# Kernel optimization log

Measured on AMD Instinct MI355X. Metric: run time of the kernel, lower is better.

## Reference

```python
import jax, jax.numpy as jnp
import numpy as np

SIM_T = 32  # simulation_length


def uniform_spikes(rates, T):
    """Faithful port of to_uniform_spikes, vectorized over all T cycles.
    rates: (B, D) in [0,1] -> spike train (T, B, D) of {0,1} floats."""
    N = jnp.round(rates * T).astype(jnp.int32)          # (B, D)
    cycles = jnp.arange(T, dtype=jnp.float32)[:, None, None]  # (T,1,1)
    N_safe = jnp.maximum(N, 1)
    spacing = T / N_safe.astype(jnp.float32)
    mask = (N != 0) & (N != T)                          # cycle < T always holds here
    res = mask & (jnp.floor(cycles / spacing) < N_safe) & (jnp.floor(jnp.mod(cycles, spacing)) == 0)
    res = res.astype(jnp.float32)
    res = jnp.where(N == T, jnp.float32(1.0), res)      # result[N == T] = 1.0
    return res


def lif_core(spikes_in, weight, threshold):
    """LIF integration: memb += inp @ W.T; fired = threshold < memb; Default reset.
    spikes_in: (T, B, in); weight: (out, in). Returns (T, B, out) spike train."""
    B = spikes_in.shape[1]
    out_dim = weight.shape[0]

    def step(memb, s):
        memb = memb + s @ weight.T
        fired = threshold < memb                        # thresholding_mode '<'
        memb = jnp.where(fired, memb - threshold, memb) # firing_mode 'Default'
        return memb, fired.astype(jnp.float32)

    _, out_train = jax.lax.scan(step, jnp.zeros((B, out_dim), spikes_in.dtype), spikes_in)
    return out_train


def setup_inputs() -> dict:
    key = jax.random.key(0)
    k = jax.random.split(key, 8)
    B, D_in = 64, 4096
    x = jax.random.uniform(k[0], (B, D_in), dtype=jnp.float32)          # rates in [0,1]
    w0 = jax.random.normal(k[1], (4096, 4096), dtype=jnp.float32) / np.sqrt(4096.0)
    t0 = jnp.float32(1.0)
    w2 = jax.random.normal(k[2], (1000, 1024), dtype=jnp.float32) / np.sqrt(1024.0)
    t2 = jnp.float32(1.0)
    idx0 = jax.random.permutation(k[3], 4096).astype(jnp.int32)
    idx1 = jax.random.permutation(k[4], 4096).astype(jnp.int32)
    idx2 = jax.random.permutation(k[5], 1024).astype(jnp.int32)
    idx_out = jnp.arange(1000, dtype=jnp.int32)
    return {"x": x, "w0": w0, "t0": t0, "w2": w2, "t2": t2,
            "idx0": idx0, "idx1": idx1, "idx2": idx2, "idx_out": idx_out}


def reference(x, w0, t0, w2, t2, idx0, idx1, idx2, idx_out):
    B = x.shape[0]
    T = SIM_T
    # Input encoding (Uniform spike mode), train shape (T, B, 4096)
    inp_train = uniform_spikes(x, T)
    # NeuralCore 0: per-source gather + LIF
    s0 = lif_core(inp_train[:, :, idx0], w0, t0)        # (T, B, 4096)
    # ComputeOp avg_pool2d: sync barrier -> rates over full window
    rates = s0[:, :, idx1].mean(axis=0)                 # (B, 4096)
    C, H, W = 64, 8, 8
    xr = rates.reshape(B, C, H, W)
    pooled = xr.reshape(B, C, H // 2, 2, W // 2, 2).mean(axis=(3, 5))  # (B, 64, 4, 4)
    y_rates = jnp.clip(pooled.reshape(B, -1), 0.0, 1.0) # (B, 1024)
    s1 = uniform_spikes(y_rates, T)                     # (T, B, 1024)
    # NeuralCore 2
    s2 = lif_core(s1[:, :, idx2], w2, t2)               # (T, B, 1000)
    # Output accumulation over cycles (spike counts)
    return s2[:, :, idx_out].sum(axis=0)                # (B, 1000)
```

## Files before the change

kernel.cpp:

```cpp
#include <hip/hip_runtime.h>
#include <stdint.h>
#include <stddef.h>

#define D0 4096
#define D1 1024
#define NOUT 1000
#define NB 64
#define PD0 4352
#define PD1 1264

constexpr uint32_t spike_pattern_ct(int N) {
  if (N <= 0) return 0u;
  if (N >= 32) return 0xFFFFFFFFu;
  float sp = 32.0f / (float)N;
  uint32_t m = 0;
  for (int c = 0; c < 32; ++c) {
    double q = (double)c / (double)sp;
    int n = (int)q;
    double r = (double)c - (double)n * (double)sp;
    if (r < 1.0) m |= (1u << c);
  }
  return m;
}

__global__ void transpose_w0_k(const float* __restrict__ w, float* __restrict__ wt) {
  __shared__ float tile[32][33];
  int j0 = blockIdx.x * 32;
  int o0 = blockIdx.y * 32;
  int tx = threadIdx.x, ty = threadIdx.y;
  float4 v = *reinterpret_cast<const float4*>(&w[(size_t)(o0 + ty) * D0 + j0 + 4 * tx]);
  tile[ty][4 * tx + 0] = v.x;
  tile[ty][4 * tx + 1] = v.y;
  tile[ty][4 * tx + 2] = v.z;
  tile[ty][4 * tx + 3] = v.w;
  __syncthreads();
  float4 u;
  u.x = tile[4 * tx + 0][ty];
  u.y = tile[4 * tx + 1][ty];
  u.z = tile[4 * tx + 2][ty];
  u.w = tile[4 * tx + 3][ty];
  *reinterpret_cast<float4*>(&wt[(size_t)(j0 + ty) * D0 + o0 + 4 * tx]) = u;
}

__global__ void transpose_w2_k(const float* __restrict__ w, float* __restrict__ wt) {
  __shared__ float tile[32][33];
  int j0 = blockIdx.x * 32;
  int o0 = blockIdx.y * 32;
  int tx = threadIdx.x, ty = threadIdx.y;
  int o = o0 + ty;
  float4 v = make_float4(0.f, 0.f, 0.f, 0.f);
  if (o < NOUT) v = *reinterpret_cast<const float4*>(&w[(size_t)o * D1 + j0 + 4 * tx]);
  tile[ty][4 * tx + 0] = v.x;
  tile[ty][4 * tx + 1] = v.y;
  tile[ty][4 * tx + 2] = v.z;
  tile[ty][4 * tx + 3] = v.w;
  __syncthreads();
  float4 u;
  u.x = tile[4 * tx + 0][ty];
  u.y = tile[4 * tx + 1][ty];
  u.z = tile[4 * tx + 2][ty];
  u.w = tile[4 * tx + 3][ty];
  *reinterpret_cast<float4*>(&wt[(size_t)(j0 + ty) * D1 + o0 + 4 * tx]) = u;
}

__global__ void prep_sort0_k(const float* __restrict__ x, const int* __restrict__ idx0,
                             uint16_t* __restrict__ perm, int* __restrict__ starts) {
  __shared__ int keys[D0];
  __shared__ int hist[33];
  __shared__ int base[34];
  __shared__ int cursor[33];
  int b = blockIdx.x;
  int tid = threadIdx.x;
  if (tid < 33) hist[tid] = 0;
  for (int p = tid; p < PD0; p += 256) perm[(size_t)b * PD0 + p] = 0;
  __syncthreads();
  for (int j = tid; j < D0; j += 256) {
    int k = (int)rintf(x[b * D0 + idx0[j]] * 32.0f);
    keys[j] = k;
    atomicAdd(&hist[k], 1);
  }
  __syncthreads();
  if (tid == 0) {
    int s = 0;
    for (int k = 0; k < 33; ++k) {
      base[k] = s; cursor[k] = s;
      s = (s + hist[k] + 7) & ~7;
    }
    base[33] = s;
  }
  __syncthreads();
  if (tid < 34) starts[b * 68 + tid] = base[tid];
  if (tid < 33) starts[b * 68 + 34 + tid] = hist[tid];
  for (int j = tid; j < D0; j += 256) {
    int k = keys[j];
    int pos = atomicAdd(&cursor[k], 1);
    perm[(size_t)b * PD0 + pos] = (uint16_t)j;
  }
}

__global__ void prep_sort1_k(const int* __restrict__ k0, const int* __restrict__ idx1,
                             const int* __restrict__ idx2,
                             uint16_t* __restrict__ perm, int* __restrict__ starts) {
  __shared__ int keys[D1];
  __shared__ int hist[33];
  __shared__ int base[34];
  __shared__ int cursor[33];
  int b = blockIdx.x;
  int tid = threadIdx.x;
  if (tid < 33) hist[tid] = 0;
  for (int p = tid; p < PD1; p += 256) perm[(size_t)b * PD1 + p] = 0;
  __syncthreads();
  for (int j = tid; j < D1; j += 256) {
    int q2 = idx2[j];
    int c = q2 >> 4;
    int h2 = (q2 >> 2) & 3;
    int w2 = q2 & 3;
    int cnt = 0;
#pragma unroll
    for (int dh = 0; dh < 2; ++dh)
#pragma unroll
      for (int dw = 0; dw < 2; ++dw) {
        int q = c * 64 + (2 * h2 + dh) * 8 + (2 * w2 + dw);
        cnt += k0[b * D0 + idx1[q]];
      }
    int k = (int)rintf((float)cnt * 0.25f);
    keys[j] = k;
    atomicAdd(&hist[k], 1);
  }
  __syncthreads();
  if (tid == 0) {
    int s = 0;
    for (int k = 0; k < 33; ++k) {
      base[k] = s; cursor[k] = s;
      s = (s + hist[k] + 7) & ~7;
    }
    base[33] = s;
  }
  __syncthreads();
  if (tid < 34) starts[b * 68 + tid] = base[tid];
  if (tid < 33) starts[b * 68 + 34 + tid] = hist[tid];
  for (int j = tid; j < D1; j += 256) {
    int k = keys[j];
    int pos = atomicAdd(&cursor[k], 1);
    perm[(size_t)b * PD1 + pos] = (uint16_t)j;
  }
}

template <int D, int PD, int OSTRIDE, int TILES>
__launch_bounds__(512, 2)
__global__ void lif_core_k(const float* __restrict__ wt, const uint16_t* __restrict__ perm,
                           const int* __restrict__ starts, const float* __restrict__ thr_p,
                           int* __restrict__ cnt_out) {
  __shared__ double cshare[16][256];
  __shared__ uint16_t permS[PD];
  int tid = threadIdx.x;
  int b = blockIdx.y;
  int col = tid & 255;
  int half = __builtin_amdgcn_readfirstlane(tid >> 8);

  {
    const ushort2* p2 = reinterpret_cast<const ushort2*>(perm + (size_t)b * PD);
    ushort2* s2 = reinterpret_cast<ushort2*>(permS);
    for (int i = tid; i < PD / 2; i += 512) s2[i] = p2[i];
  }
  __syncthreads();

  const int* stA = starts + b * 68;
  const int* stL = starts + b * 68 + 34;
  double th = (double)thr_p[0];

#define RDIDX(P) do { \
    const uint32_t* _q = reinterpret_cast<const uint32_t*>(permS + ip); \
    uint32_t _w0 = _q[0], _w1 = _q[1], _w2 = _q[2], _w3 = _q[3]; \
    uint32_t _s0 = __builtin_amdgcn_readfirstlane(_w0); \
    uint32_t _s1 = __builtin_amdgcn_readfirstlane(_w1); \
    uint32_t _s2 = __builtin_amdgcn_readfirstlane(_w2); \
    uint32_t _s3 = __builtin_amdgcn_readfirstlane(_w3); \
    P##0 = _s0 & 0xffffu; P##1 = _s0 >> 16; \
    P##2 = _s1 & 0xffffu; P##3 = _s1 >> 16; \
    P##4 = _s2 & 0xffffu; P##5 = _s2 >> 16; \
    P##6 = _s3 & 0xffffu; P##7 = _s3 >> 16; \
    ip += 8; \
  } while (0)

#define GATHER(F, P) do { \
    F##0 = wt[(size_t)P##0 * OSTRIDE + o]; \
    F##1 = wt[(size_t)P##1 * OSTRIDE + o]; \
    F##2 = wt[(size_t)P##2 * OSTRIDE + o]; \
    F##3 = wt[(size_t)P##3 * OSTRIDE + o]; \
    F##4 = wt[(size_t)P##4 * OSTRIDE + o]; \
    F##5 = wt[(size_t)P##5 * OSTRIDE + o]; \
    F##6 = wt[(size_t)P##6 * OSTRIDE + o]; \
    F##7 = wt[(size_t)P##7 * OSTRIDE + o]; \
  } while (0)

#define ACC8(F) do { \
    a0 += (double)F##0; a1 += (double)F##1; a2 += (double)F##2; a3 += (double)F##3; \
    a0 += (double)F##4; a1 += (double)F##5; a2 += (double)F##6; a3 += (double)F##7; \
  } while (0)

  for (int zt = 0; zt < TILES; ++zt) {
    int o = (blockIdx.x + gridDim.x * zt) * 256 + col;

    double bs[33];
#pragma unroll
    for (int k = 1; k <= 32; ++k) bs[k] = 0.0;

#pragma unroll
    for (int k = 1; k <= 32; ++k) {
      int hs0 = __builtin_amdgcn_readfirstlane(stA[k]);
      int len = __builtin_amdgcn_readfirstlane(stL[k]);
      if (len == 0) continue;
      int half_lo = ((len >> 1) + 7) & ~7;
      int mid8 = half_lo < len ? half_lo : len;
      int ip  = half ? hs0 + mid8 : hs0;
      int myn = half ? len - mid8 : mid8;
      if (myn == 0) continue;
      int ng = myn >> 3, rem = myn & 7;
      uint32_t pA0, pA1, pA2, pA3, pA4, pA5, pA6, pA7;
      uint32_t pB0, pB1, pB2, pB3, pB4, pB5, pB6, pB7;
      float fA0, fA1, fA2, fA3, fA4, fA5, fA6, fA7;
      float fB0, fB1, fB2, fB3, fB4, fB5, fB6, fB7;
      double a0 = 0.0, a1 = 0.0, a2 = 0.0, a3 = 0.0;
      if (ng > 0) {
        RDIDX(pA); GATHER(fA, pA);
        int g = 1;
        for (; g + 1 < ng; g += 2) {
          RDIDX(pB); GATHER(fB, pB);
          ACC8(fA);
          RDIDX(pA); GATHER(fA, pA);
          ACC8(fB);
        }
        if (g < ng) {
          RDIDX(pB); GATHER(fB, pB);
          ACC8(fA);
          ACC8(fB);
        } else {
          ACC8(fA);
        }
      }
      if (rem) {
        RDIDX(pA); GATHER(fA, pA);
        a0 += (double)fA0;
        if (rem > 1) a1 += (double)fA1;
        if (rem > 2) a2 += (double)fA2;
        if (rem > 3) a3 += (double)fA3;
        if (rem > 4) a0 += (double)fA4;
        if (rem > 5) a1 += (double)fA5;
        if (rem > 6) a2 += (double)fA6;
      }
      bs[k] = (a0 + a1) + (a2 + a3);
    }

    __syncthreads();
    if (half) {
#pragma unroll
      for (int k = 1; k <= 16; ++k) cshare[k - 1][col] = bs[k];
    }
    __syncthreads();
    if (!half) {
#pragma unroll
      for (int k = 1; k <= 16; ++k) bs[k] += cshare[k - 1][col];
    }
    __syncthreads();
    if (half) {
#pragma unroll
      for (int k = 17; k <= 32; ++k) cshare[k - 17][col] = bs[k];
    }
    __syncthreads();
    if (!half) {
#pragma unroll
      for (int k = 17; k <= 32; ++k) bs[k] += cshare[k - 17][col];

      double memb = 0.0;
      int cnt = 0;
#pragma unroll
      for (int t = 0; t < 32; ++t) {
#pragma unroll
        for (int k = 1; k <= 32; ++k)
          if ((spike_pattern_ct(k) >> t) & 1u) memb += bs[k];
        if (memb > th) { memb -= th; ++cnt; }
      }
      cnt_out[(size_t)b * OSTRIDE + o] = cnt;
    }
  }
#undef RDIDX
#undef GATHER
#undef ACC8
}

__global__ void write_out_k(const int* __restrict__ cnt2, const int* __restrict__ idx_out,
                            float* __restrict__ out) {
  int i = blockIdx.x * 256 + threadIdx.x;
  if (i >= NB * NOUT) return;
  int b = i / NOUT;
  int r = i - b * NOUT;
  out[i] = (float)cnt2[b * D1 + idx_out[r]];
}

extern "C" void kernel_launch(void* const* d_in, const int* in_sizes, int n_in,
                              void* d_out, int out_size, void* d_ws, size_t ws_size,
                              hipStream_t stream) {
  const float* x      = (const float*)d_in[0];
  const float* w0     = (const float*)d_in[1];
  const float* t0     = (const float*)d_in[2];
  const float* w2     = (const float*)d_in[3];
  const float* t2     = (const float*)d_in[4];
  const int*   idx0   = (const int*)d_in[5];
  const int*   idx1   = (const int*)d_in[6];
  const int*   idx2   = (const int*)d_in[7];
  const int*   idx_out= (const int*)d_in[8];
  float* out = (float*)d_out;

  char* ws = (char*)d_ws;
  float*    w0T    = (float*)ws;    ws += (size_t)D0 * D0 * 4;
  float*    w2T    = (float*)ws;    ws += (size_t)D1 * D1 * 4;
  uint16_t* perm0  = (uint16_t*)ws; ws += (size_t)NB * PD0 * 2;
  uint16_t* perm2  = (uint16_t*)ws; ws += (size_t)NB * PD1 * 2;
  int*      k0     = (int*)ws;      ws += (size_t)NB * D0 * 4;
  int*      cnt2   = (int*)ws;      ws += (size_t)NB * D1 * 4;
  int*      starts0= (int*)ws;      ws += (size_t)NB * 68 * 4;
  int*      starts2= (int*)ws;      ws += (size_t)NB * 68 * 4;

  transpose_w0_k<<<dim3(D0 / 32, D0 / 32), dim3(8, 32), 0, stream>>>(w0, w0T);
  transpose_w2_k<<<dim3(D1 / 32, D1 / 32), dim3(8, 32), 0, stream>>>(w2, w2T);
  prep_sort0_k<<<NB, 256, 0, stream>>>(x, idx0, perm0, starts0);
  lif_core_k<D0, PD0, D0, 2><<<dim3(8, NB, 1), 512, 0, stream>>>(w0T, perm0, starts0, t0, k0);
  prep_sort1_k<<<NB, 256, 0, stream>>>(k0, idx1, idx2, perm2, starts2);
  lif_core_k<D1, PD1, D1, 1><<<dim3(4, NB, 1), 512, 0, stream>>>(w2T, perm2, starts2, t2, cnt2);
  write_out_k<<<(NB * NOUT + 255) / 256, 256, 0, stream>>>(cnt2, idx_out, out);
}
```

Baseline: 384.9 us.

## Split LIF buckets across four thread groups in 1024-thread blocks

The LIF kernel blocks grow from 512 to 1024 threads, organised as four 256-thread groups. Each group now owns 8 of the 32 spike-count buckets outright, instead of two halves splitting every bucket's index range. Per-thread partial sums shrink from 33 doubles to 8, and the four-barrier two-phase exchange becomes a single shared-memory write. Group 0 then reads the other groups' sums directly from shared memory during the threshold loop. The aim is lower register pressure and more waves in flight for the latency-bound gather, at the cost of load imbalance between groups, larger shared memory, and a very aggressive launch-bounds occupancy hint that may force register spills.

New measurement: 361.6 us. 6.1% less time.

```diff
diff --git a/kernel.cpp b/kernel.cpp
--- a/kernel.cpp
+++ b/kernel.cpp
@@ -147,21 +147,21 @@
 }
 
 template <int D, int PD, int OSTRIDE, int TILES>
-__launch_bounds__(512, 2)
+__launch_bounds__(1024, 8)
 __global__ void lif_core_k(const float* __restrict__ wt, const uint16_t* __restrict__ perm,
                            const int* __restrict__ starts, const float* __restrict__ thr_p,
                            int* __restrict__ cnt_out) {
-  __shared__ double cshare[16][256];
+  __shared__ double cshare[24][256];
   __shared__ uint16_t permS[PD];
   int tid = threadIdx.x;
   int b = blockIdx.y;
   int col = tid & 255;
-  int half = __builtin_amdgcn_readfirstlane(tid >> 8);
+  int g = __builtin_amdgcn_readfirstlane(tid >> 8);
 
   {
     const ushort2* p2 = reinterpret_cast<const ushort2*>(perm + (size_t)b * PD);
     ushort2* s2 = reinterpret_cast<ushort2*>(permS);
-    for (int i = tid; i < PD / 2; i += 512) s2[i] = p2[i];
+    for (int i = tid; i < PD / 2; i += 1024) s2[i] = p2[i];
   }
   __syncthreads();
 
@@ -202,21 +202,18 @@
   for (int zt = 0; zt < TILES; ++zt) {
     int o = (blockIdx.x + gridDim.x * zt) * 256 + col;
 
-    double bs[33];
-#pragma unroll
-    for (int k = 1; k <= 32; ++k) bs[k] = 0.0;
-
-#pragma unroll
-    for (int k = 1; k <= 32; ++k) {
+    double bs[8];
+#pragma unroll
+    for (int i = 0; i < 8; ++i) bs[i] = 0.0;
+
+#pragma unroll
+    for (int i = 0; i < 8; ++i) {
+      int k = 4 * i + g + 1;
       int hs0 = __builtin_amdgcn_readfirstlane(stA[k]);
       int len = __builtin_amdgcn_readfirstlane(stL[k]);
       if (len == 0) continue;
-      int half_lo = ((len >> 1) + 7) & ~7;
-      int mid8 = half_lo < len ? half_lo : len;
-      int ip  = half ? hs0 + mid8 : hs0;
-      int myn = half ? len - mid8 : mid8;
-      if (myn == 0) continue;
-      int ng = myn >> 3, rem = myn & 7;
+      int ip = hs0;
+      int ng = len >> 3, rem = len & 7;
       uint32_t pA0, pA1, pA2, pA3, pA4, pA5, pA6, pA7;
       uint32_t pB0, pB1, pB2, pB3, pB4, pB5, pB6, pB7;
       float fA0, fA1, fA2, fA3, fA4, fA5, fA6, fA7;
@@ -224,14 +221,14 @@
       double a0 = 0.0, a1 = 0.0, a2 = 0.0, a3 = 0.0;
       if (ng > 0) {
         RDIDX(pA); GATHER(fA, pA);
-        int g = 1;
-        for (; g + 1 < ng; g += 2) {
+        int gg = 1;
+        for (; gg + 1 < ng; gg += 2) {
           RDIDX(pB); GATHER(fB, pB);
           ACC8(fA);
           RDIDX(pA); GATHER(fA, pA);
           ACC8(fB);
         }
-        if (g < ng) {
+        if (gg < ng) {
           RDIDX(pB); GATHER(fB, pB);
           ACC8(fA);
           ACC8(fB);
@@ -249,36 +246,29 @@
         if (rem > 5) a1 += (double)fA5;
         if (rem > 6) a2 += (double)fA6;
       }
-      bs[k] = (a0 + a1) + (a2 + a3);
+      bs[i] = (a0 + a1) + (a2 + a3);
     }
 
     __syncthreads();
-    if (half) {
-#pragma unroll
-      for (int k = 1; k <= 16; ++k) cshare[k - 1][col] = bs[k];
+    if (g > 0) {
+#pragma unroll
+      for (int i = 0; i < 8; ++i) cshare[(g - 1) * 8 + i][col] = bs[i];
     }
     __syncthreads();
-    if (!half) {
-#pragma unroll
-      for (int k = 1; k <= 16; ++k) bs[k] += cshare[k - 1][col];
-    }
-    __syncthreads();
-    if (half) {
-#pragma unroll
-      for (int k = 17; k <= 32; ++k) cshare[k - 17][col] = bs[k];
-    }
-    __syncthreads();
-    if (!half) {
-#pragma unroll
-      for (int k = 17; k <= 32; ++k) bs[k] += cshare[k - 17][col];
-
+    if (g == 0) {
       double memb = 0.0;
       int cnt = 0;
 #pragma unroll
       for (int t = 0; t < 32; ++t) {
 #pragma unroll
         for (int k = 1; k <= 32; ++k)
-          if ((spike_pattern_ct(k) >> t) & 1u) memb += bs[k];
+          if ((spike_pattern_ct(k) >> t) & 1u) {
+            constexpr_int:;
+            const int gi = (k - 1) & 3;
+            const int ii = (k - 1) >> 2;
+            double v = (gi == 0) ? bs[ii] : cshare[(gi - 1) * 8 + ii][col];
+            memb += v;
+          }
         if (memb > th) { memb -= th; ++cnt; }
       }
       cnt_out[(size_t)b * OSTRIDE + o] = cnt;
@@ -325,8 +315,8 @@
   transpose_w0_k<<<dim3(D0 / 32, D0 / 32), dim3(8, 32), 0, stream>>>(w0, w0T);
   transpose_w2_k<<<dim3(D1 / 32, D1 / 32), dim3(8, 32), 0, stream>>>(w2, w2T);
   prep_sort0_k<<<NB, 256, 0, stream>>>(x, idx0, perm0, starts0);
-  lif_core_k<D0, PD0, D0, 2><<<dim3(8, NB, 1), 512, 0, stream>>>(w0T, perm0, starts0, t0, k0);
+  lif_core_k<D0, PD0, D0, 2><<<dim3(8, NB, 1), 1024, 0, stream>>>(w0T, perm0, starts0, t0, k0);
   prep_sort1_k<<<NB, 256, 0, stream>>>(k0, idx1, idx2, perm2, starts2);
-  lif_core_k<D1, PD1, D1, 1><<<dim3(4, NB, 1), 512, 0, stream>>>(w2T, perm2, starts2, t2, cnt2);
+  lif_core_k<D1, PD1, D1, 1><<<dim3(4, NB, 1), 1024, 0, stream>>>(w2T, perm2, starts2, t2, cnt2);
   write_out_k<<<(NB * NOUT + 255) / 256, 256, 0, stream>>>(cnt2, idx_out, out);
 }
```
